# Kernel tuning notes

Hardware: AMD Instinct MI355X
Metric: run time of the kernel (lower is better)

## Reference

```python
import jax, jax.numpy as jnp
import numpy as np

N = 50000
E = 100000
D = 768


def setup_inputs() -> dict:
    key = jax.random.key(0)
    ks = jax.random.split(key, 8)
    x = jax.random.normal(ks[0], (N, D), dtype=jnp.float32)
    edge_index = jax.random.randint(ks[1], (2, E), 0, N, dtype=jnp.int64)
    s = 1.0 / np.sqrt(D)
    W1l = jax.random.uniform(ks[2], (D, D), jnp.float32, -s, s)
    b1l = jax.random.uniform(ks[3], (D,), jnp.float32, -s, s)
    W1r = jax.random.uniform(ks[4], (D, D), jnp.float32, -s, s)
    W2l = jax.random.uniform(ks[5], (D, D), jnp.float32, -s, s)
    b2l = jax.random.uniform(ks[6], (D,), jnp.float32, -s, s)
    W2r = jax.random.uniform(ks[7], (D, D), jnp.float32, -s, s)
    return {"x": x, "edge_index": edge_index, "W1l": W1l, "b1l": b1l,
            "W1r": W1r, "W2l": W2l, "b2l": b2l, "W2r": W2r}


def sage_conv(x, src, dst, Wl, bl, Wr):
    # mean-aggregate neighbor (source) features at target nodes
    summed = jax.ops.segment_sum(x[src], dst, num_segments=N)  # [N, D]
    deg = jax.ops.segment_sum(jnp.ones((src.shape[0],), x.dtype), dst,
                              num_segments=N)
    agg = summed / jnp.clip(deg, 1.0)[:, None]
    # lin_l(agg) + lin_r(x)  (PyG SAGEConv: lin_l has bias, lin_r does not)
    return agg @ Wl.T + bl + x @ Wr.T


def reference(x, edge_index, W1l, b1l, W1r, W2l, b2l, W2r):
    src, dst = edge_index[0], edge_index[1]
    h = sage_conv(x, src, dst, W1l, b1l, W1r)
    h = jax.nn.relu(h)
    return sage_conv(h, src, dst, W2l, b2l, W2r)
```

## Files before the change

kernel.cpp:

```cpp
#include <hip/hip_runtime.h>
#include <stdint.h>

#define NN 50000
#define NE 100000
#define DD 768
#define KC 1536
#define SCAN_B 196
#define NTM 391
#define NTN 6

typedef __attribute__((ext_vector_type(8))) __bf16 bf16x8;
typedef __attribute__((ext_vector_type(4))) float floatx4;

static __device__ __forceinline__ float bf2f(unsigned short u) {
    union { unsigned int u; float f; } c; c.u = ((unsigned int)u) << 16; return c.f;
}
static __device__ __forceinline__ unsigned short f2bf(float f) {
    union { float f; unsigned int u; } c; c.f = f;
    return (unsigned short)((c.u + 0x7FFFu + ((c.u >> 16) & 1u)) >> 16);
}

static __device__ __forceinline__ void gld16(const void* g, void* l) {
    __builtin_amdgcn_global_load_lds(
        (const __attribute__((address_space(1))) unsigned int*)g,
        (__attribute__((address_space(3))) unsigned int*)l, 16, 0, 0);
}


__global__ __launch_bounds__(192) void k_convert_x(const float* __restrict__ x,
                                                   unsigned short* __restrict__ acat) {
    const int n = blockIdx.x;
    const int c = threadIdx.x * 4;
    const float4 v = *(const float4*)(x + (size_t)n * DD + c);
    ushort4 o;
    o.x = f2bf(v.x); o.y = f2bf(v.y); o.z = f2bf(v.z); o.w = f2bf(v.w);
    *(ushort4*)(acat + (size_t)n * KC + DD + c) = o;
}

__global__ __launch_bounds__(384) void k_convert_w(const float* __restrict__ W1l,
                                                   const float* __restrict__ W1r,
                                                   const float* __restrict__ W2l,
                                                   const float* __restrict__ W2r,
                                                   unsigned short* __restrict__ B1,
                                                   unsigned short* __restrict__ B2) {
    const int j = blockIdx.x;
    const int layer = blockIdx.y;
    const int k = threadIdx.x * 4;
    const float* Wl = layer ? W2l : W1l;
    const float* Wr = layer ? W2r : W1r;
    unsigned short* B = layer ? B2 : B1;
    const float4 v = (k < DD) ? *(const float4*)(Wl + (size_t)j * DD + k)
                              : *(const float4*)(Wr + (size_t)j * DD + (k - DD));
    ushort4 o; o.x = f2bf(v.x); o.y = f2bf(v.y); o.z = f2bf(v.z); o.w = f2bf(v.w);
    *(ushort4*)(B + (size_t)j * KC + k) = o;
}


__global__ __launch_bounds__(256) void k_hist(const int* __restrict__ dst,
                                              int* __restrict__ cnt) {
    int e = blockIdx.x * 256 + threadIdx.x;
    if (e < NE) atomicAdd(&cnt[dst[e]], 1);
}

__global__ __launch_bounds__(256) void k_scan1(const int* __restrict__ cnt,
                                               int* __restrict__ rowptr,
                                               int* __restrict__ partial) {
    __shared__ int buf[256];
    const int t = threadIdx.x;
    const int i = blockIdx.x * 256 + t;
    int v = (i < NN) ? cnt[i] : 0;
    buf[t] = v;
    __syncthreads();
#pragma unroll
    for (int off = 1; off < 256; off <<= 1) {
        int u = (t >= off) ? buf[t - off] : 0;
        __syncthreads();
        buf[t] += u;
        __syncthreads();
    }
    if (i < NN) rowptr[i + 1] = buf[t];
    if (t == 255) partial[blockIdx.x] = buf[255];
}

__global__ __launch_bounds__(256) void k_scan2(int* __restrict__ partial) {
    __shared__ int buf[256];
    const int t = threadIdx.x;
    int v = (t < SCAN_B) ? partial[t] : 0;
    buf[t] = v;
    __syncthreads();
#pragma unroll
    for (int off = 1; off < 256; off <<= 1) {
        int u = (t >= off) ? buf[t - off] : 0;
        __syncthreads();
        buf[t] += u;
        __syncthreads();
    }
    if (t < SCAN_B) partial[t] = buf[t] - v;
}

__global__ __launch_bounds__(256) void k_scan3(int* __restrict__ rowptr,
                                               const int* __restrict__ partial) {
    const int i = blockIdx.x * 256 + threadIdx.x;
    if (i < NN) rowptr[i + 1] += partial[blockIdx.x];
    if (i == 0) rowptr[0] = 0;
}

__global__ __launch_bounds__(256) void k_fill(const int* __restrict__ src,
                                              const int* __restrict__ dst,
                                              const int* __restrict__ rowptr,
                                              int* __restrict__ cursor,
                                              int* __restrict__ esrc) {
    int e = blockIdx.x * 256 + threadIdx.x;
    if (e < NE) {
        const int d = dst[e];
        const int pos = atomicAdd(&cursor[d], 1);
        esrc[rowptr[d] + pos] = src[e];
    }
}

__global__ __launch_bounds__(192) void k_agg(const unsigned short* __restrict__ srcmat,
                                             const int* __restrict__ rowptr,
                                             const int* __restrict__ esrc,
                                             unsigned short* __restrict__ dstmat) {
    const int n = blockIdx.x;
    const int c = threadIdx.x * 4;
    const int beg = rowptr[n], end = rowptr[n + 1];
    float4 a = {0.f, 0.f, 0.f, 0.f};
    for (int e = beg; e < end; ++e) {
        const int s = esrc[e];
        const ushort4 v = *(const ushort4*)(srcmat + (size_t)s * KC + DD + c);
        a.x += bf2f(v.x); a.y += bf2f(v.y); a.z += bf2f(v.z); a.w += bf2f(v.w);
    }
    const float inv = (end > beg) ? 1.0f / (float)(end - beg) : 1.0f;
    ushort4 o;
    o.x = f2bf(a.x * inv); o.y = f2bf(a.y * inv);
    o.z = f2bf(a.z * inv); o.w = f2bf(a.w * inv);
    *(ushort4*)(dstmat + (size_t)n * KC + c) = o;
}

template <int MODE>
__global__ __launch_bounds__(256) void k_gemm(const unsigned short* __restrict__ A,
                                              const unsigned short* __restrict__ B,
                                              const float* __restrict__ bias,
                                              unsigned short* __restrict__ outA,
                                              float* __restrict__ outF) {
    __shared__ alignas(16) unsigned short sA[2][128 * 32];
    __shared__ alignas(16) unsigned short sB[2][128 * 32];
    const int tid = threadIdx.x;
    const int w = tid >> 6, lane = tid & 63;
    const int quad = lane >> 4, r16 = lane & 15;
    const int wm = (w & 1) * 64, wn = (w >> 1) * 64;

    const int nwg = NTM * NTN;
    const int q = nwg >> 3, r = nwg & 7;
    const int xcd = blockIdx.x & 7, slot = blockIdx.x >> 3;
    const int L = (xcd < r ? xcd * (q + 1) : r * (q + 1) + (xcd - r) * q) + slot;
    const int tn = L % NTN;
    const int tm = L / NTN;
    const int rowBase = tm * 128;

    floatx4 acc[4][4];
#pragma unroll
    for (int i = 0; i < 4; ++i)
#pragma unroll
        for (int j = 0; j < 4; ++j) acc[i][j] = (floatx4){0.f, 0.f, 0.f, 0.f};

    auto stage = [&](int buf, int kt) {
        const int k0 = kt * 32;
#pragma unroll
        for (int qq = 0; qq < 2; ++qq) {
            const int c0 = (w * 2 + qq) * 64;
            const int c = c0 + lane;
            const int row = c >> 2;
            const int col = (c & 3) * 8;
            int gr = rowBase + row; if (gr > NN - 1) gr = NN - 1;
            gld16(A + (size_t)gr * KC + k0 + col, &sA[buf][(size_t)c0 * 8]);
            gld16(B + (size_t)(tn * 128 + row) * KC + k0 + col, &sB[buf][(size_t)c0 * 8]);
        }
    };

    const int nk = KC / 32;
    int cur = 0;
    stage(0, 0);
    __syncthreads();

    for (int kt = 0; kt < nk; ++kt) {
        if (kt + 1 < nk) stage(cur ^ 1, kt + 1);
        bf16x8 af[4], bfr[4];
#pragma unroll
        for (int i = 0; i < 4; ++i)
            af[i] = *(const bf16x8*)(&sA[cur][(wm + i * 16 + r16) * 32 + quad * 8]);
#pragma unroll
        for (int j = 0; j < 4; ++j)
            bfr[j] = *(const bf16x8*)(&sB[cur][(wn + j * 16 + r16) * 32 + quad * 8]);
#pragma unroll
        for (int i = 0; i < 4; ++i)
#pragma unroll
            for (int j = 0; j < 4; ++j)
                acc[i][j] = __builtin_amdgcn_mfma_f32_16x16x32_bf16(af[i], bfr[j], acc[i][j], 0, 0, 0);
        __syncthreads();
        cur ^= 1;
    }

#pragma unroll
    for (int i = 0; i < 4; ++i)
#pragma unroll
        for (int j = 0; j < 4; ++j) {
            const int gcol = tn * 128 + wn + j * 16 + r16;
            const float bv = bias[gcol];
#pragma unroll
            for (int rr = 0; rr < 4; ++rr) {
                const int grow = rowBase + wm + i * 16 + quad * 4 + rr;
                if (grow < NN) {
                    float v = acc[i][j][rr] + bv;
                    if (MODE == 0) {
                        v = fmaxf(v, 0.0f);
                        outA[(size_t)grow * KC + DD + gcol] = f2bf(v);
                    } else {
                        outF[(size_t)grow * DD + gcol] = v;
                    }
                }
            }
        }
}

extern "C" void kernel_launch(void* const* d_in, const int* in_sizes, int n_in,
                              void* d_out, int out_size, void* d_ws, size_t ws_size,
                              hipStream_t stream) {
    const float* x   = (const float*)d_in[0];
    const int*   ei  = (const int*)d_in[1];
    const float* W1l = (const float*)d_in[2];
    const float* b1l = (const float*)d_in[3];
    const float* W1r = (const float*)d_in[4];
    const float* W2l = (const float*)d_in[5];
    const float* b2l = (const float*)d_in[6];
    const float* W2r = (const float*)d_in[7];
    const int* src = ei;
    const int* dst = ei + NE;
    float* out = (float*)d_out;

    char* ws = (char*)d_ws;
    unsigned short* Acat1 = (unsigned short*)ws;
    unsigned short* Acat2 = (unsigned short*)(ws + (size_t)NN * KC * 2);
    unsigned short* B1    = (unsigned short*)(ws + (size_t)NN * KC * 4);
    unsigned short* B2    = B1 + (size_t)DD * KC;
    int* cnt    = (int*)(ws + (size_t)NN * KC * 4 + (size_t)DD * KC * 4);
    int* rowptr = cnt + NN;
    int* esrc   = rowptr + NN + 1;
    int* partial = esrc + NE;

    hipMemsetAsync(cnt, 0, NN * sizeof(int), stream);
    k_hist<<<(NE + 255) / 256, 256, 0, stream>>>(dst, cnt);
    k_scan1<<<SCAN_B, 256, 0, stream>>>(cnt, rowptr, partial);
    k_scan2<<<1, 256, 0, stream>>>(partial);
    k_scan3<<<SCAN_B, 256, 0, stream>>>(rowptr, partial);
    hipMemsetAsync(cnt, 0, NN * sizeof(int), stream);
    k_fill<<<(NE + 255) / 256, 256, 0, stream>>>(src, dst, rowptr, cnt, esrc);

    k_convert_x<<<NN, 192, 0, stream>>>(x, Acat1);
    dim3 wgrid(DD, 2);
    k_convert_w<<<wgrid, 384, 0, stream>>>(W1l, W1r, W2l, W2r, B1, B2);

    const int ggrid = NTM * NTN;

    k_agg<<<NN, 192, 0, stream>>>(Acat1, rowptr, esrc, Acat1);
    k_gemm<0><<<ggrid, 256, 0, stream>>>(Acat1, B1, b1l, Acat2, nullptr);

    k_agg<<<NN, 192, 0, stream>>>(Acat2, rowptr, esrc, Acat2);
    k_gemm<1><<<ggrid, 256, 0, stream>>>(Acat2, B2, b2l, nullptr, out);
}
```

Before: 773.5 us.

## Swizzle LDS tile layout and hoist GEMM staging address math

The GEMM mainloop now XOR-swizzles the 16-byte column chunk of each row in the LDS tiles, applied both when staging loads and when reading fragments. The aim is to cut LDS bank conflicts on the bf16x8 fragment reads. Per-thread global pointers are computed once and bumped by 32 elements per k-step instead of being recomputed. The loop is also unrolled by two with fixed buffer indices, which removes the dynamic buffer toggle. The swizzle must match exactly between write and read, and the loop assumes nk is even.

```diff
diff --git a/kernel.cpp b/kernel.cpp
--- a/kernel.cpp
+++ b/kernel.cpp
@@ -165,41 +165,58 @@
 #pragma unroll
         for (int j = 0; j < 4; ++j) acc[i][j] = (floatx4){0.f, 0.f, 0.f, 0.f};
 
-    auto stage = [&](int buf, int kt) {
-        const int k0 = kt * 32;
+    const unsigned short* aP[2];
+    const unsigned short* bP[2];
+    int c0q[2];
+#pragma unroll
+    for (int qq = 0; qq < 2; ++qq) {
+        const int c0 = (w * 2 + qq) * 64;
+        const int c = c0 + lane;
+        const int row = c >> 2;
+        const int colSwz = ((c & 3) ^ ((c >> 3) & 3)) * 8;
+        int gr = rowBase + row; if (gr > NN - 1) gr = NN - 1;
+        aP[qq] = A + (size_t)gr * KC + colSwz;
+        bP[qq] = B + (size_t)(tn * 128 + row) * KC + colSwz;
+        c0q[qq] = c0;
+    }
+
+    auto stage = [&](int buf) {
 #pragma unroll
         for (int qq = 0; qq < 2; ++qq) {
-            const int c0 = (w * 2 + qq) * 64;
-            const int c = c0 + lane;
-            const int row = c >> 2;
-            const int col = (c & 3) * 8;
-            int gr = rowBase + row; if (gr > NN - 1) gr = NN - 1;
-            gld16(A + (size_t)gr * KC + k0 + col, &sA[buf][(size_t)c0 * 8]);
-            gld16(B + (size_t)(tn * 128 + row) * KC + k0 + col, &sB[buf][(size_t)c0 * 8]);
+            gld16(aP[qq], &sA[buf][(size_t)c0q[qq] * 8]);
+            gld16(bP[qq], &sB[buf][(size_t)c0q[qq] * 8]);
         }
+        aP[0] += 32; aP[1] += 32; bP[0] += 32; bP[1] += 32;
     };
 
-    const int nk = KC / 32;
-    int cur = 0;
-    stage(0, 0);
-    __syncthreads();
-
-    for (int kt = 0; kt < nk; ++kt) {
-        if (kt + 1 < nk) stage(cur ^ 1, kt + 1);
+    const int qs = (quad ^ ((r16 >> 1) & 3)) * 8;
+
+    auto compute = [&](int buf) {
         bf16x8 af[4], bfr[4];
 #pragma unroll
         for (int i = 0; i < 4; ++i)
-            af[i] = *(const bf16x8*)(&sA[cur][(wm + i * 16 + r16) * 32 + quad * 8]);
+            af[i] = *(const bf16x8*)(&sA[buf][(wm + i * 16 + r16) * 32 + qs]);
 #pragma unroll
         for (int j = 0; j < 4; ++j)
-            bfr[j] = *(const bf16x8*)(&sB[cur][(wn + j * 16 + r16) * 32 + quad * 8]);
+            bfr[j] = *(const bf16x8*)(&sB[buf][(wn + j * 16 + r16) * 32 + qs]);
 #pragma unroll
         for (int i = 0; i < 4; ++i)
 #pragma unroll
             for (int j = 0; j < 4; ++j)
                 acc[i][j] = __builtin_amdgcn_mfma_f32_16x16x32_bf16(af[i], bfr[j], acc[i][j], 0, 0, 0);
-        __syncthreads();
-        cur ^= 1;
+    };
+
+    const int nk = KC / 32;
+    stage(0);
+    __syncthreads();
+
+    for (int kt = 0; kt < nk; kt += 2) {
+        if (kt + 1 < nk) stage(1);
+        compute(0);
+        __syncthreads();
+        if (kt + 2 < nk) stage(0);
+        compute(1);
+        __syncthreads();
     }
 
 #pragma unroll
```

Measured after the change: 802.9 us. +3.8%, slower.

## Restructure GEMM to 128x256x64 tiles with triple-buffered XOR-swizzled LDS pipeline

Applied to the files above, without the earlier changes.

Widens the GEMM tile to 128x256 with BK=64 and 512 threads, halving the N tile count. It also triple-buffers LDS with XOR-swizzled columns to avoid bank conflicts, and splits each K step into two phases that interleave global-to-LDS loads with MFMA work, using explicit vmcnt waits, barriers and setprio. The aim is to hide memory latency and raise data reuse per tile. In exchange it uses more LDS (144KB), which limits occupancy, and it hardcodes the K-loop count for KC=1536.

```diff
diff --git a/kernel.cpp b/kernel.cpp
--- a/kernel.cpp
+++ b/kernel.cpp
@@ -6,8 +6,11 @@
 #define DD 768
 #define KC 1536
 #define SCAN_B 196
+#define BM 128
+#define BN 256
+#define BK 64
 #define NTM 391
-#define NTN 6
+#define NTN 3
 
 typedef __attribute__((ext_vector_type(8))) __bf16 bf16x8;
 typedef __attribute__((ext_vector_type(4))) float floatx4;
@@ -139,17 +142,18 @@
 }
 
 template <int MODE>
-__global__ __launch_bounds__(256) void k_gemm(const unsigned short* __restrict__ A,
+__global__ __launch_bounds__(512) void k_gemm(const unsigned short* __restrict__ A,
                                               const unsigned short* __restrict__ B,
                                               const float* __restrict__ bias,
                                               unsigned short* __restrict__ outA,
                                               float* __restrict__ outF) {
-    __shared__ alignas(16) unsigned short sA[2][128 * 32];
-    __shared__ alignas(16) unsigned short sB[2][128 * 32];
+    __shared__ alignas(16) unsigned short sA[3][BM * BK];
+    __shared__ alignas(16) unsigned short sB[3][BN * BK];
     const int tid = threadIdx.x;
     const int w = tid >> 6, lane = tid & 63;
     const int quad = lane >> 4, r16 = lane & 15;
-    const int wm = (w & 1) * 64, wn = (w >> 1) * 64;
+    const int wr = w >> 2, wc = w & 3;
+    const int wm = wr * 64, wn = wc * 64;
 
     const int nwg = NTM * NTN;
     const int q = nwg >> 3, r = nwg & 7;
@@ -157,7 +161,7 @@
     const int L = (xcd < r ? xcd * (q + 1) : r * (q + 1) + (xcd - r) * q) + slot;
     const int tn = L % NTN;
     const int tm = L / NTN;
-    const int rowBase = tm * 128;
+    const int rowBase = tm * BM;
 
     floatx4 acc[4][4];
 #pragma unroll
@@ -165,54 +169,100 @@
 #pragma unroll
         for (int j = 0; j < 4; ++j) acc[i][j] = (floatx4){0.f, 0.f, 0.f, 0.f};
 
-    auto stage = [&](int buf, int kt) {
-        const int k0 = kt * 32;
-#pragma unroll
-        for (int qq = 0; qq < 2; ++qq) {
-            const int c0 = (w * 2 + qq) * 64;
-            const int c = c0 + lane;
-            const int row = c >> 2;
-            const int col = (c & 3) * 8;
-            int gr = rowBase + row; if (gr > NN - 1) gr = NN - 1;
-            gld16(A + (size_t)gr * KC + k0 + col, &sA[buf][(size_t)c0 * 8]);
-            gld16(B + (size_t)(tn * 128 + row) * KC + k0 + col, &sB[buf][(size_t)c0 * 8]);
+    const unsigned short* aS[2];
+    const unsigned short* bS[4];
+#pragma unroll
+    for (int l = 0; l < 2; ++l) {
+        const int c = l * 512 + tid;
+        const int row = c >> 3;
+        const int jd = ((c & 7) ^ (row & 7)) * 8;
+        int gr = rowBase + row; if (gr > NN - 1) gr = NN - 1;
+        aS[l] = A + (size_t)gr * KC + jd;
+    }
+#pragma unroll
+    for (int l = 0; l < 4; ++l) {
+        const int c = l * 512 + tid;
+        const int row = c >> 3;
+        const int jd = ((c & 7) ^ (row & 7)) * 8;
+        bS[l] = B + (size_t)(tn * BN + row) * KC + jd;
+    }
+
+    auto stageK = [&](int d, int half) {
+        if (half == 0) {
+            gld16(aS[0], &sA[d][(0 * 512 + w * 64) * 8]);
+            gld16(aS[1], &sA[d][(1 * 512 + w * 64) * 8]);
+            gld16(bS[0], &sB[d][(0 * 512 + w * 64) * 8]);
+        } else {
+            gld16(bS[1], &sB[d][(1 * 512 + w * 64) * 8]);
+            gld16(bS[2], &sB[d][(2 * 512 + w * 64) * 8]);
+            gld16(bS[3], &sB[d][(3 * 512 + w * 64) * 8]);
+            aS[0] += BK; aS[1] += BK;
+            bS[0] += BK; bS[1] += BK; bS[2] += BK; bS[3] += BK;
         }
     };
 
-    const int nk = KC / 32;
-    int cur = 0;
-    stage(0, 0);
-    __syncthreads();
-
-    for (int kt = 0; kt < nk; ++kt) {
-        if (kt + 1 < nk) stage(cur ^ 1, kt + 1);
+    auto phase = [&](int s, int p, int d, int doStage) {
+        const int physc = ((p * 4 + quad) ^ (r16 & 7)) * 8;
         bf16x8 af[4], bfr[4];
 #pragma unroll
-        for (int i = 0; i < 4; ++i)
-            af[i] = *(const bf16x8*)(&sA[cur][(wm + i * 16 + r16) * 32 + quad * 8]);
-#pragma unroll
-        for (int j = 0; j < 4; ++j)
-            bfr[j] = *(const bf16x8*)(&sB[cur][(wn + j * 16 + r16) * 32 + quad * 8]);
-#pragma unroll
-        for (int i = 0; i < 4; ++i)
-#pragma unroll
-            for (int j = 0; j < 4; ++j)
-                acc[i][j] = __builtin_amdgcn_mfma_f32_16x16x32_bf16(af[i], bfr[j], acc[i][j], 0, 0, 0);
-        __syncthreads();
-        cur ^= 1;
-    }
-
-#pragma unroll
-    for (int i = 0; i < 4; ++i)
-#pragma unroll
-        for (int j = 0; j < 4; ++j) {
-            const int gcol = tn * 128 + wn + j * 16 + r16;
+        for (int mf = 0; mf < 4; ++mf)
+            af[mf] = *(const bf16x8*)(&sA[s][(wm + mf * 16 + r16) * BK + physc]);
+#pragma unroll
+        for (int nf = 0; nf < 4; ++nf)
+            bfr[nf] = *(const bf16x8*)(&sB[s][(wn + nf * 16 + r16) * BK + physc]);
+        if (doStage) stageK(d, p);
+        __builtin_amdgcn_sched_barrier(0);
+        __builtin_amdgcn_s_barrier();
+        __builtin_amdgcn_sched_barrier(0);
+        __builtin_amdgcn_s_setprio(1);
+#pragma unroll
+        for (int mf = 0; mf < 4; ++mf)
+#pragma unroll
+            for (int nf = 0; nf < 4; ++nf)
+                acc[mf][nf] = __builtin_amdgcn_mfma_f32_16x16x32_bf16(af[mf], bfr[nf], acc[mf][nf], 0, 0, 0);
+        __builtin_amdgcn_s_setprio(0);
+        __builtin_amdgcn_sched_barrier(0);
+    };
+
+#define SB                                            \
+    do {                                              \
+        __builtin_amdgcn_s_barrier();                 \
+        __builtin_amdgcn_sched_barrier(0);            \
+    } while (0)
+#define VW(N)                                             \
+    do {                                                  \
+        __builtin_amdgcn_sched_barrier(0);                \
+        asm volatile("s_waitcnt vmcnt(" #N ")" ::: "memory"); \
+    } while (0)
+
+    stageK(0, 0); stageK(0, 1);
+    stageK(1, 0); stageK(1, 1);
+    VW(6);
+    SB;
+
+#pragma unroll 1
+    for (int g = 0; g < 7; ++g) {
+        phase(0, 0, 2, 1); SB; phase(0, 1, 2, 1); VW(6); SB;
+        phase(1, 0, 0, 1); SB; phase(1, 1, 0, 1); VW(6); SB;
+        phase(2, 0, 1, 1); SB; phase(2, 1, 1, 1); VW(6); SB;
+    }
+    phase(0, 0, 2, 1); SB; phase(0, 1, 2, 1); VW(6); SB;
+    phase(1, 0, 0, 0); SB; phase(1, 1, 0, 0); VW(0); SB;
+    phase(2, 0, 0, 0); SB; phase(2, 1, 0, 0);
+#undef SB
+#undef VW
+
+#pragma unroll
+    for (int mf = 0; mf < 4; ++mf)
+#pragma unroll
+        for (int nf = 0; nf < 4; ++nf) {
+            const int gcol = tn * BN + wn + nf * 16 + r16;
             const float bv = bias[gcol];
 #pragma unroll
             for (int rr = 0; rr < 4; ++rr) {
-                const int grow = rowBase + wm + i * 16 + quad * 4 + rr;
+                const int grow = rowBase + wm + mf * 16 + quad * 4 + rr;
                 if (grow < NN) {
-                    float v = acc[i][j][rr] + bv;
+                    float v = acc[mf][nf][rr] + bv;
                     if (MODE == 0) {
                         v = fmaxf(v, 0.0f);
                         outA[(size_t)grow * KC + DD + gcol] = f2bf(v);
@@ -264,8 +314,8 @@
     const int ggrid = NTM * NTN;
 
     k_agg<<<NN, 192, 0, stream>>>(Acat1, rowptr, esrc, Acat1);
-    k_gemm<0><<<ggrid, 256, 0, stream>>>(Acat1, B1, b1l, Acat2, nullptr);
+    k_gemm<0><<<ggrid, 512, 0, stream>>>(Acat1, B1, b1l, Acat2, nullptr);
 
     k_agg<<<NN, 192, 0, stream>>>(Acat2, rowptr, esrc, Acat2);
-    k_gemm<1><<<ggrid, 256, 0, stream>>>(Acat2, B2, b2l, nullptr, out);
-}
+    k_gemm<1><<<ggrid, 512, 0, stream>>>(Acat2, B2, b2l, nullptr, out);
+}
```

After: 727.3 us. -6.0%, faster.
